# Optimization experiments

Hardware: AMD Instinct MI355X
Metric: run time of the kernel (lower is better)

## Reference

```python
import jax, jax.numpy as jnp
import numpy as np
from jax import lax

STRIDES = (8, 16, 32, 64, 128)
NUM_CONVS = 4
IN_CH = 256
NUM_CLASSES = 80
NUM_REG = 4  # reg head outputs NUM_REG + 1 channels (centerness first)
SIZES = [(128, 128), (64, 64), (32, 32), (16, 16), (8, 8)]
BATCH = 4


def _conv(x, w):
    # x: (N,C,H,W), w: (O,I,kh,kw), stride 1, SAME padding
    return lax.conv_general_dilated(x, w, (1, 1), 'SAME',
                                    dimension_numbers=('NCHW', 'OIHW', 'NCHW'))


def _head(x, conv_w, bn_scale, bn_bias, final_w, final_b):
    # Shared decoder: NUM_CONVS x (3x3 conv -> BN(eval, folded to scale/bias) -> ReLU),
    # then 1x1 pointwise conv with bias.
    for i in range(NUM_CONVS):
        x = _conv(x, conv_w[i])
        x = x * bn_scale[i][None, :, None, None] + bn_bias[i][None, :, None, None]
        x = jnp.maximum(x, 0.0)
    return _conv(x, final_w) + final_b[None, :, None, None]


def setup_inputs() -> dict:
    key = jax.random.key(0)
    ks = jax.random.split(key, 16)
    inp = {}
    for i, (h, w) in enumerate(SIZES):
        inp[f'fpn{i}'] = jax.random.normal(ks[i], (BATCH, IN_CH, h, w), dtype=jnp.float32)
    wstd = 0.02
    inp['cls_conv_w'] = jax.random.normal(ks[5], (NUM_CONVS, IN_CH, IN_CH, 3, 3), dtype=jnp.float32) * wstd
    inp['cls_bn_scale'] = jnp.ones((NUM_CONVS, IN_CH), dtype=jnp.float32) + 0.1 * jax.random.normal(ks[6], (NUM_CONVS, IN_CH), dtype=jnp.float32)
    inp['cls_bn_bias'] = 0.1 * jax.random.normal(ks[7], (NUM_CONVS, IN_CH), dtype=jnp.float32)
    inp['cls_final_w'] = jax.random.normal(ks[8], (NUM_CLASSES, IN_CH, 1, 1), dtype=jnp.float32) * wstd
    # prior-prob bias init: -log((1-0.01)/0.01)
    inp['cls_final_b'] = jnp.full((NUM_CLASSES,), -float(np.log(99.0)), dtype=jnp.float32)
    inp['reg_conv_w'] = jax.random.normal(ks[9], (NUM_CONVS, IN_CH, IN_CH, 3, 3), dtype=jnp.float32) * wstd
    inp['reg_bn_scale'] = jnp.ones((NUM_CONVS, IN_CH), dtype=jnp.float32) + 0.1 * jax.random.normal(ks[10], (NUM_CONVS, IN_CH), dtype=jnp.float32)
    inp['reg_bn_bias'] = 0.1 * jax.random.normal(ks[11], (NUM_CONVS, IN_CH), dtype=jnp.float32)
    inp['reg_final_w'] = jax.random.normal(ks[12], (NUM_REG + 1, IN_CH, 1, 1), dtype=jnp.float32) * wstd
    inp['reg_final_b'] = jax.random.normal(ks[13], (NUM_REG + 1,), dtype=jnp.float32) * 0.1
    return inp


def reference(fpn0, fpn1, fpn2, fpn3, fpn4,
              cls_conv_w, cls_bn_scale, cls_bn_bias, cls_final_w, cls_final_b,
              reg_conv_w, reg_bn_scale, reg_bn_bias, reg_final_w, reg_final_b):
    fpn = (fpn0, fpn1, fpn2, fpn3, fpn4)
    cls = tuple(_head(x, cls_conv_w, cls_bn_scale, cls_bn_bias, cls_final_w, cls_final_b) for x in fpn)
    raw = tuple(_head(x, reg_conv_w, reg_bn_scale, reg_bn_bias, reg_final_w, reg_final_b) for x in fpn)
    centerness = tuple(r[:, 0:1, :, :] for r in raw)
    reg = tuple(jnp.maximum(r[:, 1:, :, :] * float(s), 0.0) for r, s in zip(raw, STRIDES))
    # flatten (cls_list, reg_list, centerness_list) into one tuple of 15 arrays
    return cls + reg + centerness
```

## Files before the change

kernel.cpp:

```cpp
#include <hip/hip_runtime.h>

typedef __attribute__((ext_vector_type(8))) short short8;
typedef __attribute__((ext_vector_type(4))) float f32x4;

#define ACT_P 23384064ul
#define WSTEP 589824

__device__ unsigned short g_actC[ACT_P];
__device__ unsigned short g_actA0[ACT_P];
__device__ unsigned short g_actB0[ACT_P];
__device__ unsigned short g_actA1[ACT_P];
__device__ unsigned short g_actB1[ACT_P];
__device__ unsigned short g_wc[4 * WSTEP];
__device__ unsigned short g_wr[4 * WSTEP];
__device__ unsigned short g_w1c[80 * 256];

__constant__ int      C_W[5]    = {128, 64, 32, 16, 8};
__constant__ int      C_WP[5]   = {130, 66, 34, 18, 10};
__constant__ int      C_HWP[5]  = {16900, 4356, 1156, 324, 100};
__constant__ int      C_LW[5]   = {7, 6, 5, 4, 3};
__constant__ int      C_LXT[5]  = {4, 3, 2, 1, 0};
__constant__ int      C_PREF[5] = {0, 128, 160, 168, 170};
__constant__ int      C_HW[5]   = {16384, 4096, 1024, 256, 64};
__constant__ unsigned C_LOFFP[5]= {0u, 17305600u, 21766144u, 22949888u, 23281664u};
__constant__ unsigned C_CLSO[5] = {0u, 5242880u, 6553600u, 6881280u, 6963200u};
__constant__ unsigned C_REGO[5] = {6983680u, 7245824u, 7311360u, 7327744u, 7331840u};
__constant__ unsigned C_CENTO[5]= {7332864u, 7398400u, 7414784u, 7418880u, 7419904u};
__constant__ float    C_STRF[5] = {8.f, 16.f, 32.f, 64.f, 128.f};

static __device__ __forceinline__ unsigned short f2bf(float f) {
    unsigned u = __float_as_uint(f);
    unsigned r = (u + 0x7FFFu + ((u >> 16) & 1u)) >> 16;
    return (unsigned short)r;
}
static __device__ __forceinline__ float bf2f(unsigned short b) {
    return __uint_as_float(((unsigned)b) << 16);
}

#define GLOAD(dst, ptr) \
    asm volatile("global_load_dwordx4 %0, %1, off" : "=v"(dst) : "v"(ptr))

__global__ __launch_bounds__(256) void cvt_w3(
    const float* __restrict__ wc, const float* __restrict__ wr,
    unsigned short* __restrict__ oc, unsigned short* __restrict__ orr)
{
    const int co = blockIdx.x, sm = blockIdx.y, head = blockIdx.z;
    const int step = sm / 9, tap = sm - step * 9;
    const int ci = threadIdx.x;
    const float* w = head ? wr : wc;
    unsigned short* o = head ? orr : oc;
    o[(((size_t)sm * 32 + (ci >> 3)) * 256 + co) * 8 + (ci & 7)] =
        f2bf(w[(((size_t)step * 256 + co) * 256 + ci) * 9 + tap]);
}

__global__ __launch_bounds__(256) void cvt_w1(
    const float* __restrict__ w, unsigned short* __restrict__ o)
{
    for (int idx = threadIdx.x; idx < 80 * 256; idx += 256)
        o[idx] = f2bf(w[idx]);
}

__global__ __launch_bounds__(256) void zero_halo(
    unsigned short* c, unsigned short* a0, unsigned short* b0,
    unsigned short* a1, unsigned short* b1)
{
    unsigned short* bufs[5] = {c, a0, b0, a1, b1};
    const int bid = blockIdx.x;
    const int buf = bid / 20, r = bid - buf * 20, lvl = r >> 2, n = r & 3;
    const int Wp = C_WP[lvl], Hp = Wp;
    unsigned short* base = bufs[buf] + C_LOFFP[lvl] + (size_t)n * C_HWP[lvl] * 256;
    const int hc = 2 * Wp + 2 * (Hp - 2);
    uint4 z; z.x = z.y = z.z = z.w = 0u;
    for (int idx = threadIdx.x; idx < hc * 32; idx += 256) {
        int pos = idx >> 5, q = idx & 31;
        int row, col;
        if (pos < 2 * Wp) { row = (pos >= Wp) ? (Hp - 1) : 0; col = (pos >= Wp) ? pos - Wp : pos; }
        else { int rem = pos - 2 * Wp; row = 1 + (rem >> 1); col = (rem & 1) ? (Wp - 1) : 0; }
        *(uint4*)(base + ((size_t)(row * Wp + col) << 8) + q * 8) = z;
    }
}

__global__ __launch_bounds__(256) void cvt_in(
    const float* __restrict__ f0, const float* __restrict__ f1,
    const float* __restrict__ f2, const float* __restrict__ f3,
    const float* __restrict__ f4, unsigned short* __restrict__ dstC)
{
    const int lvl = blockIdx.y, n = blockIdx.z;
    const int HW = C_HW[lvl];
    const int p0 = blockIdx.x * 64;
    if (p0 >= HW) return;
    const int W = C_W[lvl], lw = C_LW[lvl], Wp = C_WP[lvl];
    const float* fp[5] = {f0, f1, f2, f3, f4};
    const float* src = fp[lvl] + (size_t)n * 256 * HW;
    unsigned short* dst = dstC + C_LOFFP[lvl] + (size_t)n * C_HWP[lvl] * 256;
    const int tid = threadIdx.x;
    __shared__ float ts[64][65];

    for (int cc = 0; cc < 256; cc += 64) {
        for (int idx = tid; idx < 64 * 64; idx += 256) {
            int ci = idx >> 6, p = idx & 63;
            ts[ci][p] = src[(size_t)(cc + ci) * HW + p0 + p];
        }
        __syncthreads();
        for (int idx = tid; idx < 64 * 64; idx += 256) {
            int p = idx >> 6, ci = idx & 63;
            int gp = p0 + p, y = gp >> lw, x = gp & (W - 1);
            dst[(size_t)((y + 1) * Wp + x + 1) * 256 + cc + ci] = f2bf(ts[ci][p]);
        }
        __syncthreads();
    }
}

__global__ __launch_bounds__(512, 2) void conv3x3_mfma(
    const unsigned short* __restrict__ src0, const unsigned short* __restrict__ src1,
    unsigned short* __restrict__ dst0, unsigned short* __restrict__ dst1,
    const unsigned short* __restrict__ wt0, const unsigned short* __restrict__ wt1,
    const float* __restrict__ sc0, const float* __restrict__ bi0,
    const float* __restrict__ sc1, const float* __restrict__ bi1)
{
    int tc = blockIdx.x;
    const int lvl = (tc >= 128) + (tc >= 160) + (tc >= 168) + (tc >= 170);
    tc -= C_PREF[lvl];
    const int head = blockIdx.z >> 2, n = blockIdx.z & 3;

    const int W = C_W[lvl], H = W, Wp = C_WP[lvl];
    const int lxt = C_LXT[lvl];
    const int tx = tc & ((1 << lxt) - 1), ty = tc >> lxt;
    const int x0 = tx * 8, y0 = ty * 16;

    const unsigned short* src = head ? src1 : src0;
    unsigned short*       dst = head ? dst1 : dst0;
    const unsigned short* wt  = head ? wt1 : wt0;
    const float* sc = head ? sc1 : sc0;
    const float* bi = head ? bi1 : bi0;
    const size_t actOff = (size_t)C_LOFFP[lvl] + (size_t)n * C_HWP[lvl] * 256;
    src += actOff; dst += actOff;

    const int tid = threadIdx.x;
    const int lane = tid & 63, wid = tid >> 6;
    const int l16 = lane & 15, quad = lane >> 4;
    const int coq = wid & 3, xh = wid >> 2;
    const int cow = coq * 64, jw = xh * 4;

    __shared__ unsigned short B_s[32 * 10 * 19 * 8];
    char* Bb = (char*)B_s;

    int goff[6], ldso[6];
#pragma unroll
    for (int it = 0; it < 6; it++) {
        int slot = tid + it * 512;
        if (slot > 2879) slot = 2879;
        int g = slot & 15, p = slot >> 4;
        int y = (p * 205) >> 11;
        int x = p - y * 10;
        int gyp = y0 + y; if (gyp > Wp - 1) gyp = Wp - 1;
        goff[it] = (((gyp * Wp) + x0 + x) << 8) + g * 8;
        ldso[it] = ((g * 10 + x) * 19 + y) * 16;
    }

    f32x4 acc[4][4];
#pragma unroll
    for (int mf = 0; mf < 4; mf++)
#pragma unroll
        for (int nf = 0; nf < 4; nf++) acc[mf][nf] = (f32x4){0.f, 0.f, 0.f, 0.f};

    {
        uint4 tv[6];
#pragma unroll
        for (int it = 0; it < 6; it++) tv[it] = *(const uint4*)(src + goff[it]);
#pragma unroll
        for (int it = 0; it < 6; it++) *(uint4*)(Bb + ldso[it]) = tv[it];
    }
    __syncthreads();

#pragma unroll
    for (int ph = 0; ph < 2; ph++) {
        if (ph == 1) {
            uint4 tv[6];
#pragma unroll
            for (int it = 0; it < 6; it++) tv[it] = *(const uint4*)(src + goff[it] + 128);
#pragma unroll
            for (int it = 0; it < 6; it++) *(uint4*)(Bb + ldso[it] + 48640) = tv[it];
            __syncthreads();
        }

        short8 Af[4][4];
        short8 Bf[2][6];

        auto wAddr = [&](int T, int mf) -> const unsigned short* {
            const int c4 = T / 9, tap = T - 9 * c4;
            const int c32 = ph * 4 + c4;
            return wt + (((tap * 32 + c32 * 4 + quad) * 256) + cow + mf * 16 + l16) * 8;
        };
        auto loadB = [&](int g, short8* dB) {
            const int c4 = g / 3, kh = g - 3 * c4;
            const int c32 = ph * 4 + c4;
#pragma unroll
            for (int j = 0; j < 6; j++)
                dB[j] = *(const short8*)(Bb +
                    (((c32 * 4 + quad) * 10 + jw + j) * 19 + l16 + kh) * 16);
        };

#pragma unroll
        for (int t = 0; t < 3; t++)
#pragma unroll
            for (int mf = 0; mf < 4; mf++) GLOAD(Af[t][mf], wAddr(t, mf));
        loadB(0, Bf[0]);

#pragma unroll
        for (int T = 0; T < 36; T++) {
            const int g = T / 3, kw = T - g * 3;
            if (T + 3 < 36) {
#pragma unroll
                for (int mf = 0; mf < 4; mf++)
                    GLOAD(Af[(T + 3) & 3][mf], wAddr(T + 3, mf));
            }
            if (kw == 0 && g + 1 < 12) loadB(g + 1, Bf[(g + 1) & 1]);
            if (T + 3 < 36)      asm volatile("s_waitcnt vmcnt(12)" ::: "memory");
            else if (T + 2 < 36) asm volatile("s_waitcnt vmcnt(8)" ::: "memory");
            else if (T + 1 < 36) asm volatile("s_waitcnt vmcnt(4)" ::: "memory");
            else                 asm volatile("s_waitcnt vmcnt(0)" ::: "memory");
            __builtin_amdgcn_sched_barrier(0);
            const short8* Ac = Af[T & 3];
            const short8* Bc = Bf[g & 1];
#pragma unroll
            for (int nf = 0; nf < 4; nf++)
#pragma unroll
                for (int mf = 0; mf < 4; mf++)
                    acc[mf][nf] = __builtin_amdgcn_mfma_f32_16x16x32_bf16(
                        Ac[mf], Bc[nf + kw], acc[mf][nf], 0, 0, 0);
        }
    }

    const int gy = y0 + l16;
    if (gy < H) {
#pragma unroll
        for (int mf = 0; mf < 4; mf++) {
            const int co4 = cow + mf * 16 + quad * 4;
            const f32x4 s4 = *(const f32x4*)(sc + co4);
            const f32x4 b4 = *(const f32x4*)(bi + co4);
#pragma unroll
            for (int nf = 0; nf < 4; nf++) {
                const int gx = x0 + jw + nf;
                f32x4 v = acc[mf][nf];
                ushort4 o;
                o.x = f2bf(fmaxf(v[0] * s4[0] + b4[0], 0.f));
                o.y = f2bf(fmaxf(v[1] * s4[1] + b4[1], 0.f));
                o.z = f2bf(fmaxf(v[2] * s4[2] + b4[2], 0.f));
                o.w = f2bf(fmaxf(v[3] * s4[3] + b4[3], 0.f));
                *(ushort4*)(dst + ((size_t)((gy + 1) * Wp + gx + 1) * 256 + co4)) = o;
            }
        }
    }
}

__global__ __launch_bounds__(256) void final_cls(
    const unsigned short* __restrict__ act, const unsigned short* __restrict__ w,
    const float* __restrict__ bias, float* __restrict__ out)
{
    const int lvl = blockIdx.y, n = blockIdx.z;
    const int HW = C_HW[lvl];
    const int p0 = blockIdx.x * 128;
    if (p0 >= HW) return;
    const int W = C_W[lvl], lw = C_LW[lvl], Wp = C_WP[lvl];

    const int tid = threadIdx.x;
    const int lane = tid & 63, wid = tid >> 6;
    const int l16 = lane & 15, quad = lane >> 4;

    const unsigned short* a = act + C_LOFFP[lvl] + (size_t)n * C_HWP[lvl] * 256;

    int px[2]; size_t aoff[2];
#pragma unroll
    for (int j = 0; j < 2; j++) {
        px[j] = p0 + wid * 32 + j * 16 + l16;
        int lpx = px[j] < HW ? px[j] : 0;
        int y = lpx >> lw, x = lpx & (W - 1);
        aoff[j] = (size_t)((y + 1) * Wp + x + 1) * 256;
    }

    f32x4 acc[5][2];
#pragma unroll
    for (int mf = 0; mf < 5; mf++) { acc[mf][0] = (f32x4){0,0,0,0}; acc[mf][1] = (f32x4){0,0,0,0}; }

    for (int cc = 0; cc < 256; cc += 32) {
        short8 b0 = *(const short8*)(a + aoff[0] + cc + quad * 8);
        short8 b1 = *(const short8*)(a + aoff[1] + cc + quad * 8);
#pragma unroll
        for (int mf = 0; mf < 5; mf++) {
            short8 av = *(const short8*)(w + (mf * 16 + l16) * 256 + cc + quad * 8);
            acc[mf][0] = __builtin_amdgcn_mfma_f32_16x16x32_bf16(av, b0, acc[mf][0], 0, 0, 0);
            acc[mf][1] = __builtin_amdgcn_mfma_f32_16x16x32_bf16(av, b1, acc[mf][1], 0, 0, 0);
        }
    }

    float* ob = out + C_CLSO[lvl] + (size_t)n * 80 * HW;
#pragma unroll
    for (int mf = 0; mf < 5; mf++) {
        const int co0 = mf * 16 + quad * 4;
#pragma unroll
        for (int j = 0; j < 2; j++) {
            if (px[j] < HW) {
#pragma unroll
                for (int r = 0; r < 4; r++)
                    ob[(size_t)(co0 + r) * HW + px[j]] = acc[mf][j][r] + bias[co0 + r];
            }
        }
    }
}

__global__ __launch_bounds__(256) void final_reg(
    const unsigned short* __restrict__ act, const float* __restrict__ w,
    const float* __restrict__ bias, float* __restrict__ out)
{
    const int lvl = blockIdx.y, n = blockIdx.z;
    const int HW = C_HW[lvl];
    const int W = C_W[lvl], lw = C_LW[lvl], Wp = C_WP[lvl];
    const int tid = threadIdx.x;

    __shared__ float ws[5 * 256];
    for (int idx = tid; idx < 5 * 256; idx += 256) ws[idx] = w[idx];
    __syncthreads();

    const int px = blockIdx.x * 256 + tid;
    if (px >= HW) return;

    const int y = px >> lw, x = px & (W - 1);
    const unsigned short* a = act + C_LOFFP[lvl] + (size_t)n * C_HWP[lvl] * 256
                            + (size_t)((y + 1) * Wp + x + 1) * 256;
    float acc[5] = {0.f, 0.f, 0.f, 0.f, 0.f};

    for (int ci = 0; ci < 256; ci += 8) {
        ushort4 u0 = *(const ushort4*)(a + ci);
        ushort4 u1 = *(const ushort4*)(a + ci + 4);
        float xv[8] = {bf2f(u0.x), bf2f(u0.y), bf2f(u0.z), bf2f(u0.w),
                       bf2f(u1.x), bf2f(u1.y), bf2f(u1.z), bf2f(u1.w)};
#pragma unroll
        for (int j = 0; j < 5; j++) {
            const float* wj = &ws[j * 256 + ci];
#pragma unroll
            for (int k = 0; k < 8; k++) acc[j] = fmaf(xv[k], wj[k], acc[j]);
        }
    }

    const float strf = C_STRF[lvl];
    out[C_CENTO[lvl] + (size_t)n * HW + px] = acc[0] + bias[0];
    float* rb = out + C_REGO[lvl] + (size_t)n * 4 * HW;
#pragma unroll
    for (int j = 0; j < 4; j++)
        rb[(size_t)j * HW + px] = fmaxf((acc[j + 1] + bias[j + 1]) * strf, 0.f);
}

extern "C" void kernel_launch(void* const* d_in, const int* in_sizes, int n_in,
                              void* d_out, int out_size, void* d_ws, size_t ws_size,
                              hipStream_t stream)
{
    const float* cls_w  = (const float*)d_in[5];
    const float* cls_s  = (const float*)d_in[6];
    const float* cls_b  = (const float*)d_in[7];
    const float* cls_fw = (const float*)d_in[8];
    const float* cls_fb = (const float*)d_in[9];
    const float* reg_w  = (const float*)d_in[10];
    const float* reg_s  = (const float*)d_in[11];
    const float* reg_b  = (const float*)d_in[12];
    const float* reg_fw = (const float*)d_in[13];
    const float* reg_fb = (const float*)d_in[14];
    float* out = (float*)d_out;

    unsigned short *actC, *actA0, *actB0, *actA1, *actB1, *wc, *wr, *w1c;
    hipGetSymbolAddress((void**)&actC,  HIP_SYMBOL(g_actC));
    hipGetSymbolAddress((void**)&actA0, HIP_SYMBOL(g_actA0));
    hipGetSymbolAddress((void**)&actB0, HIP_SYMBOL(g_actB0));
    hipGetSymbolAddress((void**)&actA1, HIP_SYMBOL(g_actA1));
    hipGetSymbolAddress((void**)&actB1, HIP_SYMBOL(g_actB1));
    hipGetSymbolAddress((void**)&wc,    HIP_SYMBOL(g_wc));
    hipGetSymbolAddress((void**)&wr,    HIP_SYMBOL(g_wr));
    hipGetSymbolAddress((void**)&w1c,   HIP_SYMBOL(g_w1c));

    cvt_w3<<<dim3(256, 36, 2), 256, 0, stream>>>(cls_w, reg_w, wc, wr);
    cvt_w1<<<1, 256, 0, stream>>>(cls_fw, w1c);
    zero_halo<<<100, 256, 0, stream>>>(actC, actA0, actB0, actA1, actB1);
    cvt_in<<<dim3(256, 5, 4), 256, 0, stream>>>(
        (const float*)d_in[0], (const float*)d_in[1], (const float*)d_in[2],
        (const float*)d_in[3], (const float*)d_in[4], actC);

    unsigned short* srcs[4][2] = {{actC, actC}, {actA0, actA1}, {actB0, actB1}, {actA0, actA1}};
    unsigned short* dsts[4][2] = {{actA0, actA1}, {actB0, actB1}, {actA0, actA1}, {actB0, actB1}};
    for (int s = 0; s < 4; s++) {
        conv3x3_mfma<<<dim3(171, 1, 8), 512, 0, stream>>>(
            srcs[s][0], srcs[s][1], dsts[s][0], dsts[s][1],
            wc + (size_t)s * WSTEP, wr + (size_t)s * WSTEP,
            cls_s + s * 256, cls_b + s * 256, reg_s + s * 256, reg_b + s * 256);
    }

    final_cls<<<dim3(128, 5, 4), 256, 0, stream>>>(actB0, w1c, cls_fb, out);
    final_reg<<<dim3(64, 5, 4), 256, 0, stream>>>(actB1, reg_fw, reg_fb, out);
}
```

Measured before the change: 1.093 ms.

## Widen conv spatial tile to 16x16 and stage input channels in halves

Doubles the conv tile width from 8 to 16 output columns, so each wave computes 8 column fragments and each weight fragment loaded from global memory is reused across twice as many MFMAs. LDS staging now holds only half the input channels at a time and restages for the second half, keeping shared memory near its old size. The tile grid halves (86 tiles per level set), the 8x8 level wastes half its tile, and occupancy drops to one block per CU because of the larger accumulator. Weight loads use immediate offsets to save address arithmetic.

```diff
diff --git a/kernel.cpp b/kernel.cpp
--- a/kernel.cpp
+++ b/kernel.cpp
@@ -19,8 +19,8 @@
 __constant__ int      C_WP[5]   = {130, 66, 34, 18, 10};
 __constant__ int      C_HWP[5]  = {16900, 4356, 1156, 324, 100};
 __constant__ int      C_LW[5]   = {7, 6, 5, 4, 3};
-__constant__ int      C_LXT[5]  = {4, 3, 2, 1, 0};
-__constant__ int      C_PREF[5] = {0, 128, 160, 168, 170};
+__constant__ int      C_LXT[5]  = {3, 2, 1, 0, 0};
+__constant__ int      C_PREF[5] = {0, 64, 80, 84, 85};
 __constant__ int      C_HW[5]   = {16384, 4096, 1024, 256, 64};
 __constant__ unsigned C_LOFFP[5]= {0u, 17305600u, 21766144u, 22949888u, 23281664u};
 __constant__ unsigned C_CLSO[5] = {0u, 5242880u, 6553600u, 6881280u, 6963200u};
@@ -37,8 +37,10 @@
     return __uint_as_float(((unsigned)b) << 16);
 }
 
-#define GLOAD(dst, ptr) \
+#define GLOAD0(dst, ptr) \
     asm volatile("global_load_dwordx4 %0, %1, off" : "=v"(dst) : "v"(ptr))
+#define GLOAD_OFF(dst, ptr, imm) \
+    asm volatile("global_load_dwordx4 %0, %1, off offset:" #imm : "=v"(dst) : "v"(ptr))
 
 __global__ __launch_bounds__(256) void cvt_w3(
     const float* __restrict__ wc, const float* __restrict__ wr,
@@ -111,7 +113,7 @@
     }
 }
 
-__global__ __launch_bounds__(512, 2) void conv3x3_mfma(
+__global__ __launch_bounds__(512, 1) void conv3x3_mfma(
     const unsigned short* __restrict__ src0, const unsigned short* __restrict__ src1,
     unsigned short* __restrict__ dst0, unsigned short* __restrict__ dst1,
     const unsigned short* __restrict__ wt0, const unsigned short* __restrict__ wt1,
@@ -119,14 +121,14 @@
     const float* __restrict__ sc1, const float* __restrict__ bi1)
 {
     int tc = blockIdx.x;
-    const int lvl = (tc >= 128) + (tc >= 160) + (tc >= 168) + (tc >= 170);
+    const int lvl = (tc >= 64) + (tc >= 80) + (tc >= 84) + (tc >= 85);
     tc -= C_PREF[lvl];
     const int head = blockIdx.z >> 2, n = blockIdx.z & 3;
 
     const int W = C_W[lvl], H = W, Wp = C_WP[lvl];
     const int lxt = C_LXT[lvl];
     const int tx = tc & ((1 << lxt) - 1), ty = tc >> lxt;
-    const int x0 = tx * 8, y0 = ty * 16;
+    const int x0 = tx * 16, y0 = ty * 16;
 
     const unsigned short* src = head ? src1 : src0;
     unsigned short*       dst = head ? dst1 : dst0;
@@ -140,81 +142,87 @@
     const int lane = tid & 63, wid = tid >> 6;
     const int l16 = lane & 15, quad = lane >> 4;
     const int coq = wid & 3, xh = wid >> 2;
-    const int cow = coq * 64, jw = xh * 4;
-
-    __shared__ unsigned short B_s[32 * 10 * 19 * 8];
+    const int cow = coq * 64, jw = xh * 8;
+
+    __shared__ unsigned short B_s[16 * 18 * 19 * 8];
     char* Bb = (char*)B_s;
 
-    int goff[6], ldso[6];
-#pragma unroll
-    for (int it = 0; it < 6; it++) {
+    int goff[11], ldso[11];
+#pragma unroll
+    for (int it = 0; it < 11; it++) {
         int slot = tid + it * 512;
-        if (slot > 2879) slot = 2879;
+        if (slot > 5183) slot = 5183;
         int g = slot & 15, p = slot >> 4;
-        int y = (p * 205) >> 11;
-        int x = p - y * 10;
+        int y = (p * 57) >> 10;
+        int x = p - y * 18;
         int gyp = y0 + y; if (gyp > Wp - 1) gyp = Wp - 1;
-        goff[it] = (((gyp * Wp) + x0 + x) << 8) + g * 8;
-        ldso[it] = ((g * 10 + x) * 19 + y) * 16;
-    }
-
-    f32x4 acc[4][4];
+        int gxp = x0 + x; if (gxp > Wp - 1) gxp = Wp - 1;
+        goff[it] = (((gyp * Wp) + gxp) << 8) + g * 8;
+        ldso[it] = ((g * 18 + x) * 19 + y) * 16;
+    }
+
+    f32x4 acc[4][8];
 #pragma unroll
     for (int mf = 0; mf < 4; mf++)
 #pragma unroll
-        for (int nf = 0; nf < 4; nf++) acc[mf][nf] = (f32x4){0.f, 0.f, 0.f, 0.f};
-
-    {
-        uint4 tv[6];
-#pragma unroll
-        for (int it = 0; it < 6; it++) tv[it] = *(const uint4*)(src + goff[it]);
-#pragma unroll
-        for (int it = 0; it < 6; it++) *(uint4*)(Bb + ldso[it]) = tv[it];
-    }
+        for (int nf = 0; nf < 8; nf++) acc[mf][nf] = (f32x4){0.f, 0.f, 0.f, 0.f};
+
+    auto stage_half = [&](int cio) {
+#pragma unroll
+        for (int rnd = 0; rnd < 2; rnd++) {
+            const int nb = rnd ? 5 : 6;
+            uint4 tv[6];
+#pragma unroll
+            for (int it = 0; it < 6; it++)
+                if (it < nb) tv[it] = *(const uint4*)(src + goff[rnd * 6 + it] + cio);
+#pragma unroll
+            for (int it = 0; it < 6; it++)
+                if (it < nb) *(uint4*)(Bb + ldso[rnd * 6 + it]) = tv[it];
+        }
+    };
+
+    stage_half(0);
     __syncthreads();
 
 #pragma unroll
     for (int ph = 0; ph < 2; ph++) {
         if (ph == 1) {
-            uint4 tv[6];
-#pragma unroll
-            for (int it = 0; it < 6; it++) tv[it] = *(const uint4*)(src + goff[it] + 128);
-#pragma unroll
-            for (int it = 0; it < 6; it++) *(uint4*)(Bb + ldso[it] + 48640) = tv[it];
             __syncthreads();
+            stage_half(128);
+            __syncthreads();
         }
 
         short8 Af[4][4];
-        short8 Bf[2][6];
-
-        auto wAddr = [&](int T, int mf) -> const unsigned short* {
+        short8 Bf[2][10];
+
+        auto wBase = [&](int T) -> const unsigned short* {
             const int c4 = T / 9, tap = T - 9 * c4;
             const int c32 = ph * 4 + c4;
-            return wt + (((tap * 32 + c32 * 4 + quad) * 256) + cow + mf * 16 + l16) * 8;
+            return wt + (((tap * 32 + c32 * 4 + quad) * 256) + cow + l16) * 8;
+        };
+        auto issueA = [&](int T, short8* dA) {
+            const unsigned short* p = wBase(T);
+            GLOAD0(dA[0], p);
+            GLOAD_OFF(dA[1], p, 256);
+            GLOAD_OFF(dA[2], p, 512);
+            GLOAD_OFF(dA[3], p, 768);
         };
         auto loadB = [&](int g, short8* dB) {
             const int c4 = g / 3, kh = g - 3 * c4;
-            const int c32 = ph * 4 + c4;
-#pragma unroll
-            for (int j = 0; j < 6; j++)
+#pragma unroll
+            for (int j = 0; j < 10; j++)
                 dB[j] = *(const short8*)(Bb +
-                    (((c32 * 4 + quad) * 10 + jw + j) * 19 + l16 + kh) * 16);
+                    (((c4 * 4 + quad) * 18 + jw + j) * 19 + l16 + kh) * 16);
         };
 
 #pragma unroll
-        for (int t = 0; t < 3; t++)
-#pragma unroll
-            for (int mf = 0; mf < 4; mf++) GLOAD(Af[t][mf], wAddr(t, mf));
+        for (int t = 0; t < 3; t++) issueA(t, Af[t]);
         loadB(0, Bf[0]);
 
 #pragma unroll
         for (int T = 0; T < 36; T++) {
             const int g = T / 3, kw = T - g * 3;
-            if (T + 3 < 36) {
-#pragma unroll
-                for (int mf = 0; mf < 4; mf++)
-                    GLOAD(Af[(T + 3) & 3][mf], wAddr(T + 3, mf));
-            }
+            if (T + 3 < 36) issueA(T + 3, Af[(T + 3) & 3]);
             if (kw == 0 && g + 1 < 12) loadB(g + 1, Bf[(g + 1) & 1]);
             if (T + 3 < 36)      asm volatile("s_waitcnt vmcnt(12)" ::: "memory");
             else if (T + 2 < 36) asm volatile("s_waitcnt vmcnt(8)" ::: "memory");
@@ -224,7 +232,7 @@
             const short8* Ac = Af[T & 3];
             const short8* Bc = Bf[g & 1];
 #pragma unroll
-            for (int nf = 0; nf < 4; nf++)
+            for (int nf = 0; nf < 8; nf++)
 #pragma unroll
                 for (int mf = 0; mf < 4; mf++)
                     acc[mf][nf] = __builtin_amdgcn_mfma_f32_16x16x32_bf16(
@@ -240,15 +248,17 @@
             const f32x4 s4 = *(const f32x4*)(sc + co4);
             const f32x4 b4 = *(const f32x4*)(bi + co4);
 #pragma unroll
-            for (int nf = 0; nf < 4; nf++) {
+            for (int nf = 0; nf < 8; nf++) {
                 const int gx = x0 + jw + nf;
-                f32x4 v = acc[mf][nf];
-                ushort4 o;
-                o.x = f2bf(fmaxf(v[0] * s4[0] + b4[0], 0.f));
-                o.y = f2bf(fmaxf(v[1] * s4[1] + b4[1], 0.f));
-                o.z = f2bf(fmaxf(v[2] * s4[2] + b4[2], 0.f));
-                o.w = f2bf(fmaxf(v[3] * s4[3] + b4[3], 0.f));
-                *(ushort4*)(dst + ((size_t)((gy + 1) * Wp + gx + 1) * 256 + co4)) = o;
+                if (gx < W) {
+                    f32x4 v = acc[mf][nf];
+                    ushort4 o;
+                    o.x = f2bf(fmaxf(v[0] * s4[0] + b4[0], 0.f));
+                    o.y = f2bf(fmaxf(v[1] * s4[1] + b4[1], 0.f));
+                    o.z = f2bf(fmaxf(v[2] * s4[2] + b4[2], 0.f));
+                    o.w = f2bf(fmaxf(v[3] * s4[3] + b4[3], 0.f));
+                    *(ushort4*)(dst + ((size_t)((gy + 1) * Wp + gx + 1) * 256 + co4)) = o;
+                }
             }
         }
     }
@@ -387,7 +397,7 @@
     unsigned short* srcs[4][2] = {{actC, actC}, {actA0, actA1}, {actB0, actB1}, {actA0, actA1}};
     unsigned short* dsts[4][2] = {{actA0, actA1}, {actB0, actB1}, {actA0, actA1}, {actB0, actB1}};
     for (int s = 0; s < 4; s++) {
-        conv3x3_mfma<<<dim3(171, 1, 8), 512, 0, stream>>>(
+        conv3x3_mfma<<<dim3(86, 1, 8), 512, 0, stream>>>(
             srcs[s][0], srcs[s][1], dsts[s][0], dsts[s][1],
             wc + (size_t)s * WSTEP, wr + (size_t)s * WSTEP,
             cls_s + s * 256, cls_b + s * 256, reg_s + s * 256, reg_b + s * 256);
```

After: 2.901 ms. 165% more time.
